# Kernel optimization log

Hardware: AMD Instinct MI355X
Metric: run time of the kernel (lower is better)

Reference implementation:

```python
import jax, jax.numpy as jnp
import numpy as np

B, N, GEO, CLS = 32, 1024, 4, 28
F0 = GEO + CLS          # 32
F1 = F0 * 2             # 64
F2 = F0 * 4             # 128
EPS = 1e-5


def _lin(x, W, b):
    return x @ W.T + b


def _bn(x, g, b):
    # torch BatchNorm1d(element_num) on [B, N, F]: channel dim is N,
    # normalize over (batch, feature) with biased variance (training mode).
    m = x.mean(axis=(0, 2), keepdims=True)
    v = ((x - m) ** 2).mean(axis=(0, 2), keepdims=True)
    return g[None, :, None] * (x - m) * jax.lax.rsqrt(v + EPS) + b[None, :, None]


def _relation(x, Wu, bu, psi, phi, wr):
    # Vectorized form of the triple python loop:
    #   S[b,i,j] = psi*phi * <x_i, x_j>, diagonal excluded
    #   out_i   = wr * (sum_j S[b,i,j] * relu(unary(x_j))) / N + x_i
    n = x.shape[1]
    U = jax.nn.relu(_lin(x, Wu, bu))                       # [B,N,F2]
    S = (psi[0] * phi[0]) * jnp.einsum('bnd,bmd->bnm', x, x)
    S = S * (1.0 - jnp.eye(n, dtype=x.dtype))              # mask i==j
    return wr[0] * (S @ U) / n + x


def setup_inputs() -> dict:
    key = jax.random.key(0)
    ks = iter(jax.random.split(key, 64))

    def W(o, i):
        return jax.random.normal(next(ks), (o, i), jnp.float32) * 0.02

    def bvec(o):
        return jnp.zeros((o,), jnp.float32)

    inp = {'input': jax.random.uniform(next(ks), (B, N, F0), jnp.float32)}
    inp.update(e1_W=W(F1, F0), e1_b=bvec(F1),
               bn1_g=jnp.ones((N,), jnp.float32), bn1_b=bvec(N),
               e2_W=W(F2, F1), e2_b=bvec(F2),
               bn2_g=jnp.ones((N,), jnp.float32), bn2_b=bvec(N),
               e3_W=W(F2, F2), e3_b=bvec(F2))
    for r in (1, 2, 3, 4):
        inp[f'r{r}_W'] = W(F2, F2)
        inp[f'r{r}_b'] = bvec(F2)
        inp[f'r{r}_psi'] = jax.random.uniform(next(ks), (1,), jnp.float32)
        inp[f'r{r}_phi'] = jax.random.uniform(next(ks), (1,), jnp.float32)
        inp[f'r{r}_wr'] = jax.random.uniform(next(ks), (1,), jnp.float32)
    inp.update(d1_W=W(F1, F2), d1_b=bvec(F1),
               dbn_g=jnp.ones((N,), jnp.float32), dbn_b=bvec(N),
               d2_W=W(F0, F1), d2_b=bvec(F0),
               bc_W=W(CLS, F0), bc_b=bvec(CLS),
               bg_W=W(GEO, F0), bg_b=bvec(GEO))
    return inp


def reference(input, e1_W, e1_b, bn1_g, bn1_b, e2_W, e2_b, bn2_g, bn2_b,
              e3_W, e3_b,
              r1_W, r1_b, r1_psi, r1_phi, r1_wr,
              r2_W, r2_b, r2_psi, r2_phi, r2_wr,
              r3_W, r3_b, r3_psi, r3_phi, r3_wr,
              r4_W, r4_b, r4_psi, r4_phi, r4_wr,
              d1_W, d1_b, dbn_g, dbn_b, d2_W, d2_b,
              bc_W, bc_b, bg_W, bg_b):
    out = jax.nn.relu(_bn(_lin(input, e1_W, e1_b), bn1_g, bn1_b))
    out = jax.nn.relu(_bn(_lin(out, e2_W, e2_b), bn2_g, bn2_b))
    enc = jax.nn.sigmoid(_lin(out, e3_W, e3_b))
    x = _relation(enc, r1_W, r1_b, r1_psi, r1_phi, r1_wr)
    x = _relation(x, r2_W, r2_b, r2_psi, r2_phi, r2_wr)
    x = _relation(x, r3_W, r3_b, r3_psi, r3_phi, r3_wr)
    x = _relation(x, r4_W, r4_b, r4_psi, r4_phi, r4_wr)
    out = jax.nn.relu(_bn(_lin(x, d1_W, d1_b), dbn_g, dbn_b))
    out = jax.nn.relu(_lin(out, d2_W, d2_b))
    syn_cls = _lin(out, bc_W, bc_b)
    syn_geo = _lin(out, bg_W, bg_b)
    return jnp.concatenate((syn_cls, syn_geo), axis=2)
```

## Files before the change

kernel.cpp:

```cpp
#include <hip/hip_runtime.h>
#include <hip/hip_bf16.h>


typedef __hip_bfloat16 bf16;
typedef unsigned short ushort_t;
typedef float v4f __attribute__((ext_vector_type(4)));
typedef short v8s __attribute__((ext_vector_type(8)));
#define MFMA_BF16 __builtin_amdgcn_mfma_f32_16x16x32_bf16

#define NB 32
#define NN 1024
#define XSTRIDE 72

__device__ __forceinline__ float ldin(const void* p, size_t i, int f32){
    return f32 ? ((const float*)p)[i] : __bfloat162float(((const bf16*)p)[i]);
}
__device__ __forceinline__ float bf2f(ushort_t u){
    return __uint_as_float((unsigned)u << 16);
}
__device__ __forceinline__ ushort_t f2bf(float v){
    bf16 h = __float2bfloat16(v);
    ushort_t s; __builtin_memcpy(&s, &h, 2);
    return s;
}
__device__ __forceinline__ void unpack8(uint4 v, float* f){
    f[0] = __uint_as_float(v.x << 16);
    f[1] = __uint_as_float(v.x & 0xffff0000u);
    f[2] = __uint_as_float(v.y << 16);
    f[3] = __uint_as_float(v.y & 0xffff0000u);
    f[4] = __uint_as_float(v.z << 16);
    f[5] = __uint_as_float(v.z & 0xffff0000u);
    f[6] = __uint_as_float(v.w << 16);
    f[7] = __uint_as_float(v.w & 0xffff0000u);
}
__device__ __forceinline__ void unpack4(uint2 v, float* f){
    f[0] = __uint_as_float(v.x << 16);
    f[1] = __uint_as_float(v.x & 0xffff0000u);
    f[2] = __uint_as_float(v.y << 16);
    f[3] = __uint_as_float(v.y & 0xffff0000u);
}

__device__ __forceinline__ int detect_dev(const void* inp){
    __shared__ int sflag;
    int t = threadIdx.x;
    if (t < 64){
        unsigned v = ((const unsigned*)inp)[t];
        unsigned long long m = __ballot((v & 0x80008000u) != 0u);
        if (t == 0) sflag = (__popcll(m) > 4) ? 1 : 0;
    }
    __syncthreads();
    return sflag;
}

struct PrepArgs {
    const void* w[9];
    int K[9], O[9], off[9];
};

__global__ __launch_bounds__(128) void k_enc0(PrepArgs a, float* __restrict__ wpf,
    ushort_t* __restrict__ whi, ushort_t* __restrict__ wlo,
    const void* __restrict__ xin,
    const void* __restrict__ e1w, const void* __restrict__ b1v,
    const void* __restrict__ g1, const void* __restrict__ bb1,
    const void* __restrict__ e2w, const void* __restrict__ b2v,
    const void* __restrict__ g2, const void* __restrict__ bb2,
    ushort_t* __restrict__ out, const void* __restrict__ detin)
{
    int f32 = detect_dev(detin);
    int t = threadIdx.x;

    #pragma unroll 1
    for (int s = 0; s < 9; s++){
        int K = a.K[s], O = a.O[s];
        int tot = (s < 4) ? K*O : 16384;
        for (int idx = blockIdx.x*128 + t; idx < tot; idx += 512*128){
            if (s < 4){
                int k = idx / O, j = idx - k*O;
                wpf[a.off[s] + idx] = ldin(a.w[s], (size_t)j*K + k, f32);
            } else {
                int n = idx >> 7, k = idx & 127;
                float v = ldin(a.w[s], (size_t)n*128 + k, f32);
                ushort_t h = f2bf(v);
                ushort_t l = f2bf(v - bf2f(h));
                int di = (s - 4)*16384 + ((k >> 3)*128 + n)*8 + (k & 7);
                whi[di] = h; wlo[di] = l;
            }
        }
    }

    __shared__ __align__(16) float wt1[32*64];
    __shared__ __align__(16) float wt2[64*128];
    __shared__ __align__(16) float xst[2][32*36];
    __shared__ __align__(16) float cst[2][64*36];
    int w = t >> 6, lane = t & 63;
    int n = blockIdx.x*2 + w;

    for (int i = t; i < 512; i += 128){
        int kq = i >> 6, j = i & 63;
        float f[4];
        if (f32){
            float4 v = *(const float4*)((const float*)e1w + (size_t)j*32 + kq*4);
            f[0]=v.x; f[1]=v.y; f[2]=v.z; f[3]=v.w;
        } else {
            uint2 v = *(const uint2*)((const ushort_t*)e1w + (size_t)j*32 + kq*4);
            unpack4(v, f);
        }
        #pragma unroll
        for (int c=0;c<4;c++) wt1[(kq*4+c)*64 + j] = f[c];
    }
    for (int i = t; i < 2048; i += 128){
        int kq = i >> 7, j = i & 127;
        float f[4];
        if (f32){
            float4 v = *(const float4*)((const float*)e2w + (size_t)j*64 + kq*4);
            f[0]=v.x; f[1]=v.y; f[2]=v.z; f[3]=v.w;
        } else {
            uint2 v = *(const uint2*)((const ushort_t*)e2w + (size_t)j*64 + kq*4);
            unpack4(v, f);
        }
        #pragma unroll
        for (int c=0;c<4;c++) wt2[(kq*4+c)*128 + j] = f[c];
    }
    for (int i = lane; i < 32*4; i += 64){
        int b = i >> 2, g = i & 3;
        float f[8];
        if (f32){
            const float* src = (const float*)xin + ((size_t)b*NN + n)*32 + g*8;
            float4 v0 = ((const float4*)src)[0];
            float4 v1 = ((const float4*)src)[1];
            f[0]=v0.x; f[1]=v0.y; f[2]=v0.z; f[3]=v0.w;
            f[4]=v1.x; f[5]=v1.y; f[6]=v1.z; f[7]=v1.w;
        } else {
            uint4 v = *(const uint4*)((const ushort_t*)xin + ((size_t)b*NN + n)*32 + (size_t)g*8);
            unpack8(v, f);
        }
        #pragma unroll
        for (int j=0;j<8;j++) xst[w][(g*8+j)*36 + b] = f[j];
    }
    __syncthreads();

    {
        int b0 = (lane & 7)*4, j0 = (lane >> 3)*8;
        float acc[4][8];
        #pragma unroll
        for (int i=0;i<4;i++)
            #pragma unroll
            for (int j=0;j<8;j++) acc[i][j] = 0.f;
        for (int k = 0; k < 32; k++){
            float xv[4], wv[8];
            *(float4*)&xv[0] = *(const float4*)&xst[w][k*36 + b0];
            *(float4*)&wv[0] = *(const float4*)&wt1[k*64 + j0];
            *(float4*)&wv[4] = *(const float4*)&wt1[k*64 + j0 + 4];
            #pragma unroll
            for (int i=0;i<4;i++)
                #pragma unroll
                for (int j=0;j<8;j++) acc[i][j] = fmaf(xv[i], wv[j], acc[i][j]);
        }
        float bj[8];
        #pragma unroll
        for (int j=0;j<8;j++) bj[j] = ldin(b1v, j0+j, f32);
        float s1 = 0.f, s2 = 0.f;
        #pragma unroll
        for (int i=0;i<4;i++)
            #pragma unroll
            for (int j=0;j<8;j++){
                float a2 = acc[i][j] + bj[j];
                acc[i][j] = a2; s1 += a2; s2 = fmaf(a2, a2, s2);
            }
        #pragma unroll
        for (int off = 32; off > 0; off >>= 1){
            s1 += __shfl_down(s1, off);
            s2 += __shfl_down(s2, off);
        }
        s1 = __shfl(s1, 0); s2 = __shfl(s2, 0);
        float m  = s1 / 2048.f;
        float vv = s2 / 2048.f - m*m;
        float rs = rsqrtf(vv + 1e-5f);
        float gv = ldin(g1, n, f32), bv = ldin(bb1, n, f32);
        #pragma unroll
        for (int i=0;i<4;i++)
            #pragma unroll
            for (int j=0;j<8;j++)
                cst[w][(j0+j)*36 + b0+i] =
                    fmaxf(fmaf(gv*(acc[i][j]-m), rs, bv), 0.f);
    }
    __syncthreads();

    {
        int b0 = (lane & 3)*8, j0 = (lane >> 2)*8;
        float acc[8][8];
        #pragma unroll
        for (int i=0;i<8;i++)
            #pragma unroll
            for (int j=0;j<8;j++) acc[i][j] = 0.f;
        for (int k = 0; k < 64; k++){
            float xv[8], wv[8];
            *(float4*)&xv[0] = *(const float4*)&cst[w][k*36 + b0];
            *(float4*)&xv[4] = *(const float4*)&cst[w][k*36 + b0 + 4];
            *(float4*)&wv[0] = *(const float4*)&wt2[k*128 + j0];
            *(float4*)&wv[4] = *(const float4*)&wt2[k*128 + j0 + 4];
            #pragma unroll
            for (int i=0;i<8;i++)
                #pragma unroll
                for (int j=0;j<8;j++) acc[i][j] = fmaf(xv[i], wv[j], acc[i][j]);
        }
        float bj[8];
        #pragma unroll
        for (int j=0;j<8;j++) bj[j] = ldin(b2v, j0+j, f32);
        float s1 = 0.f, s2 = 0.f;
        #pragma unroll
        for (int i=0;i<8;i++)
            #pragma unroll
            for (int j=0;j<8;j++){
                float a2 = acc[i][j] + bj[j];
                acc[i][j] = a2; s1 += a2; s2 = fmaf(a2, a2, s2);
            }
        #pragma unroll
        for (int off = 32; off > 0; off >>= 1){
            s1 += __shfl_down(s1, off);
            s2 += __shfl_down(s2, off);
        }
        s1 = __shfl(s1, 0); s2 = __shfl(s2, 0);
        float m  = s1 / 4096.f;
        float vv = s2 / 4096.f - m*m;
        float rs = rsqrtf(vv + 1e-5f);
        float gv = ldin(g2, n, f32), bv = ldin(bb2, n, f32);
        #pragma unroll
        for (int i=0;i<8;i++){
            union { uint4 u; ushort_t s[8]; } pk;
            #pragma unroll
            for (int j=0;j<8;j++)
                pk.s[j] = f2bf(fmaxf(fmaf(gv*(acc[i][j]-m), rs, bv), 0.f));
            *(uint4*)(out + ((size_t)(b0+i)*NN + n)*128 + j0) = pk.u;
        }
    }
}

__global__ __launch_bounds__(128) void k_dectail(
    const ushort_t* __restrict__ xin,
    const float* __restrict__ W1t,
    const void* __restrict__ d1b, const void* __restrict__ bng,
    const void* __restrict__ bnb,
    const float* __restrict__ W2t,
    const void* __restrict__ b2,
    const float* __restrict__ Wct, const void* __restrict__ bcb,
    const float* __restrict__ Wgt, const void* __restrict__ bgb,
    void* __restrict__ out, const void* __restrict__ detin)
{
    __shared__ __align__(16) float smem[8192 + 9216];
    float* wt  = smem;
    float* xst = smem + 8192;
    int f32 = detect_dev(detin);
    int t = threadIdx.x;
    int w = t >> 6, lane = t & 63;
    int n = blockIdx.x*2 + w;

    for (int i = t; i < 8192/4; i += 128)
        ((float4*)wt)[i] = ((const float4*)W1t)[i];
    float* xw = xst + w*4608;
    for (int i = lane; i < 32*16; i += 64){
        int b = i >> 4, g = i & 15;
        float f[8];
        uint4 v = *(const uint4*)(xin + ((size_t)b*NN + n)*128 + (size_t)g*8);
        unpack8(v, f);
        #pragma unroll
        for (int j=0;j<8;j++) xw[(g*8+j)*36 + b] = f[j];
    }
    __syncthreads();

    int b0 = (lane & 7)*4, j0 = (lane >> 3)*8;
    float acc[4][8];
    #pragma unroll
    for (int i=0;i<4;i++)
        #pragma unroll
        for (int j=0;j<8;j++) acc[i][j] = 0.f;
    for (int k = 0; k < 128; k++){
        float xv[4], wv[8];
        *(float4*)&xv[0] = *(const float4*)&xw[k*36 + b0];
        *(float4*)&wv[0] = *(const float4*)&wt[k*64 + j0];
        *(float4*)&wv[4] = *(const float4*)&wt[k*64 + j0 + 4];
        #pragma unroll
        for (int i=0;i<4;i++)
            #pragma unroll
            for (int j=0;j<8;j++) acc[i][j] = fmaf(xv[i], wv[j], acc[i][j]);
    }
    float bj[8];
    #pragma unroll
    for (int j=0;j<8;j++) bj[j] = ldin(d1b, j0+j, f32);
    float s1 = 0.f, s2 = 0.f;
    #pragma unroll
    for (int i=0;i<4;i++)
        #pragma unroll
        for (int j=0;j<8;j++){
            float a2 = acc[i][j] + bj[j];
            acc[i][j] = a2; s1 += a2; s2 = fmaf(a2, a2, s2);
        }
    #pragma unroll
    for (int off = 32; off > 0; off >>= 1){
        s1 += __shfl_down(s1, off);
        s2 += __shfl_down(s2, off);
    }
    s1 = __shfl(s1, 0); s2 = __shfl(s2, 0);
    float m  = s1 / 2048.f;
    float vv = s2 / 2048.f - m*m;
    float rs = rsqrtf(vv + 1e-5f);
    float gv = ldin(bng, n, f32), bv = ldin(bnb, n, f32);
    __syncthreads();

    float* w2s  = wt;
    float* wcs  = wt + 2048;
    float* wgs  = wt + 2944;
    float* cstw = xst + w*2080;
    float* hsw  = xst + 4160 + w*1056;
    for (int i = t; i < 512; i += 128) ((float4*)w2s)[i] = ((const float4*)W2t)[i];
    for (int i = t; i < 224; i += 128) ((float4*)wcs)[i] = ((const float4*)Wct)[i];
    if (t < 32) ((float4*)wgs)[t] = ((const float4*)Wgt)[t];
    #pragma unroll
    for (int i=0;i<4;i++)
        #pragma unroll
        for (int j=0;j<8;j++){
            float val = fmaxf(fmaf(gv*(acc[i][j]-m), rs, bv), 0.f);
            cstw[(b0+i)*65 + (j0+j)] = bf2f(f2bf(val));
        }
    __syncthreads();

    int b = lane & 31, jg = lane >> 5;
    float h[16];
    #pragma unroll
    for (int jj=0;jj<16;jj++) h[jj] = ldin(b2, jg*16+jj, f32);
    for (int k = 0; k < 64; k++){
        float xv = cstw[b*65 + k];
        #pragma unroll
        for (int jj=0;jj<16;jj++)
            h[jj] = fmaf(xv, w2s[k*32 + jg*16 + jj], h[jj]);
    }
    #pragma unroll
    for (int jj=0;jj<16;jj++) hsw[b*33 + jg*16 + jj] = fmaxf(h[jj], 0.f);
    __syncthreads();
    #pragma unroll
    for (int jj=0;jj<16;jj++){
        int j2 = jg*16 + jj;
        float o;
        if (j2 < 28){
            o = ldin(bcb, j2, f32);
            #pragma unroll
            for (int k=0;k<32;k++) o = fmaf(hsw[b*33 + k], wcs[k*28 + j2], o);
        } else {
            int gg = j2 - 28;
            o = ldin(bgb, gg, f32);
            #pragma unroll
            for (int k=0;k<32;k++) o = fmaf(hsw[b*33 + k], wgs[k*4 + gg], o);
        }
        size_t oi = ((size_t)b*NN + n)*32 + j2;
        if (f32) ((float*)out)[oi] = o;
        else     ((ushort_t*)out)[oi] = f2bf(o);
    }
}

__device__ __forceinline__ void tail_stage_x(ushort_t* xs, ushort_t* xt,
                                             const float o[2][16],
                                             int w, int col, int quad){
    #pragma unroll
    for (int nt=0;nt<2;nt++){
        int n = w*32 + nt*16 + col;
        #pragma unroll
        for (int m=0;m<4;m++){
            union { uint2 u2; ushort_t s[4]; } pk;
            #pragma unroll
            for (int reg=0;reg<4;reg++){
                int r = m*16 + quad*4 + reg;
                ushort_t hv = f2bf(o[nt][m*4+reg]);
                xs[((n>>3)*64 + r)*8 + (n&7)] = hv;
                pk.s[reg] = hv;
            }
            *(uint2*)&xt[n*XSTRIDE + m*16 + quad*4] = pk.u2;
        }
    }
}

__device__ __forceinline__ void tail_write_A(const ushort_t* xs, ushort_t* A,
                                             size_t row0, int t){
    uint4* dst = (uint4*)(A + row0*128);
    #pragma unroll
    for (int c = 0; c < 4; c++){
        int i = t + c*256;
        int r = i >> 4, kg = i & 15;
        dst[i] = *(const uint4*)&xs[(kg*64 + r)*8];
    }
}

__device__ __forceinline__ void mfma_hilo(const ushort_t* xs,
    const ushort_t* Bh, const ushort_t* Bl, v4f acc[4][2],
    int w, int col, int quad)
{
    #pragma unroll
    for (int m=0;m<4;m++)
        #pragma unroll
        for (int nt=0;nt<2;nt++) acc[m][nt] = (v4f){0.f,0.f,0.f,0.f};
    #pragma unroll
    for (int kt = 0; kt < 4; kt++){
        int kg = kt*4 + quad;
        v8s a[4], bh[2], bl[2];
        #pragma unroll
        for (int nt=0;nt<2;nt++){
            int n = w*32 + nt*16 + col;
            bh[nt] = *(const v8s*)&Bh[(kg*128 + n)*8];
            bl[nt] = *(const v8s*)&Bl[(kg*128 + n)*8];
        }
        #pragma unroll
        for (int m=0;m<4;m++)
            a[m] = *(const v8s*)&xs[(kg*64 + m*16 + col)*8];
        #pragma unroll
        for (int m=0;m<4;m++)
            #pragma unroll
            for (int nt=0;nt<2;nt++){
                acc[m][nt] = MFMA_BF16(a[m], bh[nt], acc[m][nt], 0, 0, 0);
                acc[m][nt] = MFMA_BF16(a[m], bl[nt], acc[m][nt], 0, 0, 0);
            }
    }
}

__device__ __forceinline__ void tail_lin_relu_T(ushort_t* xs, ushort_t* xt,
    const ushort_t* Whi, const ushort_t* Wlo, const void* bias,
    ushort_t* Tp, size_t row0, int t, int w, int col, int quad, int f32)
{
    v4f acc[4][2];
    mfma_hilo(xs, Whi, Wlo, acc, w, col, quad);
    float u[2][16];
    #pragma unroll
    for (int nt=0;nt<2;nt++){
        int n = w*32 + nt*16 + col;
        float bn = ldin(bias, n, f32);
        #pragma unroll
        for (int m=0;m<4;m++)
            #pragma unroll
            for (int reg=0;reg<4;reg++)
                u[nt][m*4+reg] = fmaxf(acc[m][nt][reg] + bn, 0.f);
    }
    __syncthreads();
    #pragma unroll
    for (int nt=0;nt<2;nt++){
        int n = w*32 + nt*16 + col;
        #pragma unroll
        for (int m=0;m<4;m++){
            union { uint2 u2; ushort_t s[4]; } pk;
            #pragma unroll
            for (int reg=0;reg<4;reg++)
                pk.s[reg] = f2bf(u[nt][m*4+reg]);
            *(uint2*)&xs[n*XSTRIDE + m*16 + quad*4] = pk.u2;
        }
    }
    __syncthreads();
    v4f tacc[4][4];
    #pragma unroll
    for (int m=0;m<4;m++)
        #pragma unroll
        for (int q=0;q<4;q++) tacc[m][q] = (v4f){0.f,0.f,0.f,0.f};
    int wn = (w & 1)*64, wc = (w >> 1)*64;
    #pragma unroll
    for (int kt = 0; kt < 2; kt++){
        int kg = kt*4 + quad;
        v8s a[4], bb[4];
        #pragma unroll
        for (int m=0;m<4;m++)
            a[m] = *(const v8s*)&xs[(wn + m*16 + col)*XSTRIDE + kg*8];
        #pragma unroll
        for (int q=0;q<4;q++)
            bb[q] = *(const v8s*)&xt[(wc + q*16 + col)*XSTRIDE + kg*8];
        #pragma unroll
        for (int m=0;m<4;m++)
            #pragma unroll
            for (int q=0;q<4;q++)
                tacc[m][q] = MFMA_BF16(a[m], bb[q], tacc[m][q], 0, 0, 0);
    }
    int s16 = (int)((row0 >> 6) & 15);
    int b   = (int)(row0 >> 10);
    ushort_t* dst = Tp + ((size_t)(s16*NB + b) << 14);
    #pragma unroll
    for (int m=0;m<4;m++)
        #pragma unroll
        for (int q=0;q<4;q++){
            int c = wc + q*16 + col;
            union { uint2 u2; ushort_t s[4]; } pk;
            #pragma unroll
            for (int reg=0;reg<4;reg++)
                pk.s[reg] = f2bf(tacc[m][q][reg]);
            *(uint2*)&dst[c*128 + wn + m*16 + quad*4] = pk.u2;
        }
}

__global__ __launch_bounds__(256) void k_linfuse0(
    const ushort_t* __restrict__ xin,
    const ushort_t* __restrict__ W3h, const ushort_t* __restrict__ W3l,
    const void* __restrict__ b3,
    const ushort_t* __restrict__ W1h, const ushort_t* __restrict__ W1l,
    const void* __restrict__ b1,
    ushort_t* __restrict__ A, ushort_t* __restrict__ Tp,
    const void* __restrict__ detin)
{
    __shared__ __align__(16) ushort_t xs[128*XSTRIDE];
    __shared__ __align__(16) ushort_t xt[128*XSTRIDE];
    int f32 = detect_dev(detin);
    int t = threadIdx.x;
    size_t row0 = (size_t)blockIdx.x * 64;
    {
        const uint4* src = (const uint4*)(xin + row0*128);
        #pragma unroll
        for (int c = 0; c < 4; c++){
            int i = t + c*256;
            int r = i >> 4, kg = i & 15;
            *(uint4*)&xs[(kg*64 + r)*8] = src[i];
        }
    }
    __syncthreads();
    int w = t >> 6, lane = t & 63;
    int col = lane & 15, quad = lane >> 4;
    v4f acc[4][2];
    mfma_hilo(xs, W3h, W3l, acc, w, col, quad);
    float o[2][16];
    #pragma unroll
    for (int nt=0;nt<2;nt++){
        int n = w*32 + nt*16 + col;
        float bn = ldin(b3, n, f32);
        #pragma unroll
        for (int m=0;m<4;m++)
            #pragma unroll
            for (int reg=0;reg<4;reg++){
                float v = acc[m][nt][reg] + bn;
                o[nt][m*4+reg] = 1.f/(1.f+expf(-v));
            }
    }
    __syncthreads();
    tail_stage_x(xs, xt, o, w, col, quad);
    __syncthreads();
    tail_write_A(xs, A, row0, t);
    tail_lin_relu_T(xs, xt, W1h, W1l, b1, Tp, row0, t, w, col, quad, f32);
}

__global__ __launch_bounds__(256) void k_tredb(const ushort_t* __restrict__ Tp,
                                               ushort_t* __restrict__ Thi, ushort_t* __restrict__ Tlo){
    int tau = blockIdx.x*256 + threadIdx.x;
    int b = tau >> 11;
    int j2 = tau & 2047;
    int cg = j2 >> 7, n = j2 & 127;
    float sum[8] = {0,0,0,0,0,0,0,0};
    #pragma unroll
    for (int s = 0; s < 16; s++){
        const ushort_t* src = Tp + ((size_t)(s*NB + b) << 14) + cg*8*128 + n;
        #pragma unroll
        for (int cc = 0; cc < 8; cc++)
            sum[cc] += bf2f(src[cc*128]);
    }
    union { uint4 u; ushort_t s[8]; } ph, pl;
    #pragma unroll
    for (int cc = 0; cc < 8; cc++){
        ushort_t h = f2bf(sum[cc]);
        ph.s[cc] = h;
        pl.s[cc] = f2bf(sum[cc] - bf2f(h));
    }
    size_t di = ((size_t)b << 14) + ((size_t)cg*128 + n)*8;
    *(uint4*)&Thi[di] = ph.u;
    *(uint4*)&Tlo[di] = pl.u;
}

template<int LAST>
__global__ __launch_bounds__(256) void k_relfuse(
    ushort_t* __restrict__ x,
    const ushort_t* __restrict__ Thi, const ushort_t* __restrict__ Tlo,
    const void* __restrict__ psi, const void* __restrict__ phi, const void* __restrict__ wr,
    const ushort_t* __restrict__ Wrh, const ushort_t* __restrict__ Wrl,
    const void* __restrict__ rbias,
    const ushort_t* __restrict__ Wnh, const ushort_t* __restrict__ Wnl,
    const void* __restrict__ bnext, ushort_t* __restrict__ Tp,
    const void* __restrict__ detin)
{
    __shared__ __align__(16) ushort_t xs[128*XSTRIDE];
    __shared__ __align__(16) ushort_t xt[128*XSTRIDE];
    __shared__ __align__(16) float sdvec[64];
    int f32 = detect_dev(detin);
    int t = threadIdx.x;
    size_t row0 = (size_t)blockIdx.x * 64;
    int b = (int)(row0 >> 10);
    {
        const uint4* src = (const uint4*)(x + row0*128);
        #pragma unroll
        for (int c = 0; c < 4; c++){
            int i = t + c*256;
            int r = i >> 4, kg = i & 15;
            *(uint4*)&xs[(kg*64 + r)*8] = src[i];
        }
    }
    __syncthreads();
    int w = t >> 6, lane = t & 63;
    int col = lane & 15, quad = lane >> 4;

    if (t < 64){
        float s = 0.f;
        #pragma unroll 8
        for (int k=0;k<128;k++){
            float v = bf2f(xs[((k>>3)*64 + t)*8 + (k&7)]);
            s = fmaf(v, v, s);
        }
        sdvec[t] = s;
    }
    {
        v4f uacc[4][2];
        mfma_hilo(xs, Wrh, Wrl, uacc, w, col, quad);
        #pragma unroll
        for (int nt=0;nt<2;nt++){
            int n = w*32 + nt*16 + col;
            float bn = ldin(rbias, n, f32);
            #pragma unroll
            for (int m=0;m<4;m++){
                union { uint2 u2; ushort_t s[4]; } pk;
                #pragma unroll
                for (int reg=0;reg<4;reg++)
                    pk.s[reg] = f2bf(fmaxf(uacc[m][nt][reg] + bn, 0.f));
                *(uint2*)&xt[n*XSTRIDE + m*16 + quad*4] = pk.u2;
            }
        }
    }
    __syncthreads();

    float alpha = ldin(wr,0,f32) * ldin(psi,0,f32) * ldin(phi,0,f32) * (1.f/1024.f);
    const ushort_t* sh = Thi + ((size_t)b << 14);
    const ushort_t* sl = Tlo + ((size_t)b << 14);
    v4f acc[4][2];
    mfma_hilo(xs, sh, sl, acc, w, col, quad);
    float o[2][16];
    #pragma unroll
    for (int m=0;m<4;m++){
        float4 d4 = *(const float4*)&sdvec[m*16 + quad*4];
        const float* dr = (const float*)&d4;
        #pragma unroll
        for (int nt=0;nt<2;nt++){
            int n = w*32 + nt*16 + col;
            #pragma unroll
            for (int reg=0;reg<4;reg++){
                int r = m*16 + quad*4 + reg;
                float ufv = bf2f(xt[n*XSTRIDE + r]);
                float xv = bf2f(xs[((n>>3)*64 + r)*8 + (n&7)]);
                o[nt][m*4+reg] = fmaf(alpha, acc[m][nt][reg] - dr[reg]*ufv, xv);
            }
        }
    }
    __syncthreads();
    tail_stage_x(xs, xt, o, w, col, quad);
    __syncthreads();
    tail_write_A(xs, x, row0, t);
    if (!LAST)
        tail_lin_relu_T(xs, xt, Wnh, Wnl, bnext, Tp,
                        row0, t, w, col, quad, f32);
}

enum { O_E1=0, O_E2=2048, O_D1=10240, O_D2=18432, O_BC=20480, O_BG=21376 };

extern "C" void kernel_launch(void* const* d_in, const int* in_sizes, int n_in,
                              void* d_out, int out_size, void* d_ws, size_t ws_size,
                              hipStream_t stream)
{
    (void)in_sizes; (void)n_in; (void)out_size; (void)ws_size;
    const void* input = d_in[0];
    const void* e1_W = d_in[1];  const void* e1_b = d_in[2];
    const void* bn1_g = d_in[3]; const void* bn1_b = d_in[4];
    const void* e2_W = d_in[5];  const void* e2_b = d_in[6];
    const void* bn2_g = d_in[7]; const void* bn2_b = d_in[8];
    const void* e3_W = d_in[9];  const void* e3_b = d_in[10];
    const void *rW[4], *rb[4], *rpsi[4], *rphi[4], *rwr[4];
    for (int r = 0; r < 4; r++){
        rW[r]   = d_in[11 + r*5 + 0];
        rb[r]   = d_in[11 + r*5 + 1];
        rpsi[r] = d_in[11 + r*5 + 2];
        rphi[r] = d_in[11 + r*5 + 3];
        rwr[r]  = d_in[11 + r*5 + 4];
    }
    const void* d1_W = d_in[31]; const void* d1_b = d_in[32];
    const void* dbn_g = d_in[33];const void* dbn_b = d_in[34];
    const void* d2_W = d_in[35]; const void* d2_b = d_in[36];
    const void* bc_W = d_in[37]; const void* bc_b = d_in[38];
    const void* bg_W = d_in[39]; const void* bg_b = d_in[40];

    float*    ws_f = (float*)d_ws;
    float*    wpf  = ws_f;
    ushort_t* whi  = (ushort_t*)(ws_f + 54272);
    ushort_t* wlo  = (ushort_t*)(ws_f + 95232);
    ushort_t* Thi  = (ushort_t*)(ws_f + 136192);
    ushort_t* Tlo  = (ushort_t*)(ws_f + 398336);
    ushort_t* Tp   = (ushort_t*)(ws_f + 660480);
    ushort_t* A    = (ushort_t*)(ws_f + 4854784);
    ushort_t* E2   = (ushort_t*)(ws_f + 9049088);

    PrepArgs pa;
    const void* srcs[9] = {d1_W, d2_W, bc_W, bg_W,
                           e3_W, rW[0], rW[1], rW[2], rW[3]};
    const int  Ks[9]   = {128,64,32,32, 128,128,128,128,128};
    const int  Os[9]   = {64,32,28,4,   128,128,128,128,128};
    const int  offs[9] = {O_D1,O_D2,O_BC,O_BG, 0,0,0,0,0};
    for (int i=0;i<9;i++){ pa.w[i]=srcs[i]; pa.K[i]=Ks[i]; pa.O[i]=Os[i]; pa.off[i]=offs[i]; }

    k_enc0<<<512, 128, 0, stream>>>(pa, wpf, whi, wlo,
                                    input, e1_W, e1_b, bn1_g, bn1_b,
                                    e2_W, e2_b, bn2_g, bn2_b,
                                    E2, input);
    k_linfuse0<<<512, 256, 0, stream>>>(E2, whi, wlo, e3_b,
                                        whi + 16384, wlo + 16384, rb[0],
                                        A, Tp, input);

    for (int r = 0; r < 4; r++){
        k_tredb<<<256, 256, 0, stream>>>(Tp, Thi, Tlo);
        if (r < 3)
            k_relfuse<0><<<512, 256, 0, stream>>>(A, Thi, Tlo,
                rpsi[r], rphi[r], rwr[r],
                whi + (size_t)(1+r)*16384, wlo + (size_t)(1+r)*16384, rb[r],
                whi + (size_t)(2+r)*16384, wlo + (size_t)(2+r)*16384, rb[r+1],
                Tp, input);
        else
            k_relfuse<1><<<512, 256, 0, stream>>>(A, Thi, Tlo,
                rpsi[r], rphi[r], rwr[r],
                whi + (size_t)4*16384, wlo + (size_t)4*16384, rb[3],
                whi, wlo, rb[0],
                Tp, input);
    }

    k_dectail<<<512, 128, 0, stream>>>(A, wpf+O_D1, d1_b, dbn_g, dbn_b,
                                       wpf+O_D2, d2_b, wpf+O_BC, bc_b,
                                       wpf+O_BG, bg_b, d_out, input);
}
```

Before: 292.4 us.

## Fuse partial-T reduction into relation kernel and drop the separate reduce pass

```diff
diff --git a/kernel.cpp b/kernel.cpp
--- a/kernel.cpp
+++ b/kernel.cpp
@@ -477,16 +477,18 @@
     int b   = (int)(row0 >> 10);
     ushort_t* dst = Tp + ((size_t)(s16*NB + b) << 14);
     #pragma unroll
-    for (int m=0;m<4;m++)
-        #pragma unroll
-        for (int q=0;q<4;q++){
-            int c = wc + q*16 + col;
-            union { uint2 u2; ushort_t s[4]; } pk;
-            #pragma unroll
-            for (int reg=0;reg<4;reg++)
-                pk.s[reg] = f2bf(tacc[m][q][reg]);
-            *(uint2*)&dst[c*128 + wn + m*16 + quad*4] = pk.u2;
-        }
+    for (int q=0;q<4;q++){
+        int c = wc + q*16 + col;
+        int cb = (c >> 3)*1024 + (c & 7);
+        #pragma unroll
+        for (int m=0;m<4;m++){
+            #pragma unroll
+            for (int reg=0;reg<4;reg++){
+                int n2 = wn + m*16 + quad*4 + reg;
+                dst[cb + n2*8] = f2bf(tacc[m][q][reg]);
+            }
+        }
+    }
 }
 
 __global__ __launch_bounds__(256) void k_linfuse0(
@@ -502,7 +504,10 @@
     __shared__ __align__(16) ushort_t xt[128*XSTRIDE];
     int f32 = detect_dev(detin);
     int t = threadIdx.x;
-    size_t row0 = (size_t)blockIdx.x * 64;
+    int bid = blockIdx.x;
+    int b   = (bid & 7) + ((bid >> 7) << 3);
+    int s16 = (bid >> 3) & 15;
+    size_t row0 = ((size_t)b*16 + s16) << 6;
     {
         const uint4* src = (const uint4*)(xin + row0*128);
         #pragma unroll
@@ -537,41 +542,16 @@
     tail_lin_relu_T(xs, xt, W1h, W1l, b1, Tp, row0, t, w, col, quad, f32);
 }
 
-__global__ __launch_bounds__(256) void k_tredb(const ushort_t* __restrict__ Tp,
-                                               ushort_t* __restrict__ Thi, ushort_t* __restrict__ Tlo){
-    int tau = blockIdx.x*256 + threadIdx.x;
-    int b = tau >> 11;
-    int j2 = tau & 2047;
-    int cg = j2 >> 7, n = j2 & 127;
-    float sum[8] = {0,0,0,0,0,0,0,0};
-    #pragma unroll
-    for (int s = 0; s < 16; s++){
-        const ushort_t* src = Tp + ((size_t)(s*NB + b) << 14) + cg*8*128 + n;
-        #pragma unroll
-        for (int cc = 0; cc < 8; cc++)
-            sum[cc] += bf2f(src[cc*128]);
-    }
-    union { uint4 u; ushort_t s[8]; } ph, pl;
-    #pragma unroll
-    for (int cc = 0; cc < 8; cc++){
-        ushort_t h = f2bf(sum[cc]);
-        ph.s[cc] = h;
-        pl.s[cc] = f2bf(sum[cc] - bf2f(h));
-    }
-    size_t di = ((size_t)b << 14) + ((size_t)cg*128 + n)*8;
-    *(uint4*)&Thi[di] = ph.u;
-    *(uint4*)&Tlo[di] = pl.u;
-}
-
 template<int LAST>
 __global__ __launch_bounds__(256) void k_relfuse(
     ushort_t* __restrict__ x,
-    const ushort_t* __restrict__ Thi, const ushort_t* __restrict__ Tlo,
+    const ushort_t* __restrict__ Tpr,
     const void* __restrict__ psi, const void* __restrict__ phi, const void* __restrict__ wr,
     const ushort_t* __restrict__ Wrh, const ushort_t* __restrict__ Wrl,
     const void* __restrict__ rbias,
     const ushort_t* __restrict__ Wnh, const ushort_t* __restrict__ Wnl,
-    const void* __restrict__ bnext, ushort_t* __restrict__ Tp,
+    const void* __restrict__ bnext,
+    ushort_t* __restrict__ Tpw,
     const void* __restrict__ detin)
 {
     __shared__ __align__(16) ushort_t xs[128*XSTRIDE];
@@ -579,8 +559,10 @@
     __shared__ __align__(16) float sdvec[64];
     int f32 = detect_dev(detin);
     int t = threadIdx.x;
-    size_t row0 = (size_t)blockIdx.x * 64;
-    int b = (int)(row0 >> 10);
+    int bid = blockIdx.x;
+    int b   = (bid & 7) + ((bid >> 7) << 3);
+    int s16 = (bid >> 3) & 15;
+    size_t row0 = ((size_t)b*16 + s16) << 6;
     {
         const uint4* src = (const uint4*)(x + row0*128);
         #pragma unroll
@@ -623,10 +605,51 @@
     __syncthreads();
 
     float alpha = ldin(wr,0,f32) * ldin(psi,0,f32) * ldin(phi,0,f32) * (1.f/1024.f);
-    const ushort_t* sh = Thi + ((size_t)b << 14);
-    const ushort_t* sl = Tlo + ((size_t)b << 14);
+    const ushort_t* Tb = Tpr + ((size_t)b << 14);
     v4f acc[4][2];
-    mfma_hilo(xs, sh, sl, acc, w, col, quad);
+    #pragma unroll
+    for (int m=0;m<4;m++)
+        #pragma unroll
+        for (int nt=0;nt<2;nt++) acc[m][nt] = (v4f){0.f,0.f,0.f,0.f};
+    #pragma unroll
+    for (int kt = 0; kt < 4; kt++){
+        int kg = kt*4 + quad;
+        v8s a[4];
+        #pragma unroll
+        for (int m=0;m<4;m++)
+            a[m] = *(const v8s*)&xs[(kg*64 + m*16 + col)*8];
+        #pragma unroll
+        for (int nt=0; nt<2; nt++){
+            int n = w*32 + nt*16 + col;
+            const ushort_t* tp0 = Tb + ((size_t)kg*128 + n)*8;
+            float sum[8] = {0.f,0.f,0.f,0.f,0.f,0.f,0.f,0.f};
+            #pragma unroll
+            for (int s = 0; s < 16; s++){
+                uint4 tv = *(const uint4*)(tp0 + ((size_t)(s*NB) << 14));
+                sum[0] += __uint_as_float(tv.x << 16);
+                sum[1] += __uint_as_float(tv.x & 0xffff0000u);
+                sum[2] += __uint_as_float(tv.y << 16);
+                sum[3] += __uint_as_float(tv.y & 0xffff0000u);
+                sum[4] += __uint_as_float(tv.z << 16);
+                sum[5] += __uint_as_float(tv.z & 0xffff0000u);
+                sum[6] += __uint_as_float(tv.w << 16);
+                sum[7] += __uint_as_float(tv.w & 0xffff0000u);
+            }
+            union { v8s v; ushort_t us[8]; } bh, bl;
+            #pragma unroll
+            for (int e=0;e<8;e++){
+                ushort_t h = f2bf(sum[e]);
+                bh.us[e] = h;
+                bl.us[e] = f2bf(sum[e] - bf2f(h));
+            }
+            #pragma unroll
+            for (int m=0;m<4;m++){
+                acc[m][nt] = MFMA_BF16(a[m], bh.v, acc[m][nt], 0, 0, 0);
+                acc[m][nt] = MFMA_BF16(a[m], bl.v, acc[m][nt], 0, 0, 0);
+            }
+        }
+    }
+
     float o[2][16];
     #pragma unroll
     for (int m=0;m<4;m++){
@@ -649,7 +672,7 @@
     __syncthreads();
     tail_write_A(xs, x, row0, t);
     if (!LAST)
-        tail_lin_relu_T(xs, xt, Wnh, Wnl, bnext, Tp,
+        tail_lin_relu_T(xs, xt, Wnh, Wnl, bnext, Tpw,
                         row0, t, w, col, quad, f32);
 }
 
@@ -684,11 +707,10 @@
     float*    wpf  = ws_f;
     ushort_t* whi  = (ushort_t*)(ws_f + 54272);
     ushort_t* wlo  = (ushort_t*)(ws_f + 95232);
-    ushort_t* Thi  = (ushort_t*)(ws_f + 136192);
-    ushort_t* Tlo  = (ushort_t*)(ws_f + 398336);
-    ushort_t* Tp   = (ushort_t*)(ws_f + 660480);
+    ushort_t* Tp0  = (ushort_t*)(ws_f + 660480);
     ushort_t* A    = (ushort_t*)(ws_f + 4854784);
     ushort_t* E2   = (ushort_t*)(ws_f + 9049088);
+    ushort_t* Tp1  = (ushort_t*)(ws_f + 11146240);
 
     PrepArgs pa;
     const void* srcs[9] = {d1_W, d2_W, bc_W, bg_W,
@@ -704,22 +726,24 @@
                                     E2, input);
     k_linfuse0<<<512, 256, 0, stream>>>(E2, whi, wlo, e3_b,
                                         whi + 16384, wlo + 16384, rb[0],
-                                        A, Tp, input);
-
+                                        A, Tp0, input);
+
+    ushort_t* tpr = Tp0;
+    ushort_t* tpw = Tp1;
     for (int r = 0; r < 4; r++){
-        k_tredb<<<256, 256, 0, stream>>>(Tp, Thi, Tlo);
         if (r < 3)
-            k_relfuse<0><<<512, 256, 0, stream>>>(A, Thi, Tlo,
+            k_relfuse<0><<<512, 256, 0, stream>>>(A, tpr,
                 rpsi[r], rphi[r], rwr[r],
                 whi + (size_t)(1+r)*16384, wlo + (size_t)(1+r)*16384, rb[r],
                 whi + (size_t)(2+r)*16384, wlo + (size_t)(2+r)*16384, rb[r+1],
-                Tp, input);
+                tpw, input);
         else
-            k_relfuse<1><<<512, 256, 0, stream>>>(A, Thi, Tlo,
+            k_relfuse<1><<<512, 256, 0, stream>>>(A, tpr,
                 rpsi[r], rphi[r], rwr[r],
                 whi + (size_t)4*16384, wlo + (size_t)4*16384, rb[3],
                 whi, wlo, rb[0],
-                Tp, input);
+                tpw, input);
+        ushort_t* tmp = tpr; tpr = tpw; tpw = tmp;
     }
 
     k_dectail<<<512, 128, 0, stream>>>(A, wpf+O_D1, d1_b, dbn_g, dbn_b,
```

Result: slower. 335.0 us (+14.6%).
